# Kernel tuning notes

Hardware: AMD Instinct MI355X
Metric: run time of the kernel (lower is better)

## Reference

```python
import jax, jax.numpy as jnp
import numpy as np

N = 1024
IN_FEATURES = 128
N_HEADS = 8
N_HIDDEN = 16  # out_features // n_heads = 128 // 8
NEG_SLOPE = 0.2


def setup_inputs() -> dict:
    key = jax.random.key(0)
    k1, k2, k3, k4, k5 = jax.random.split(key, 5)
    h = jax.random.normal(k1, (N, IN_FEATURES), dtype=jnp.float32)
    adj_mat = jax.random.randint(k2, (N, N, 1), 0, 2, dtype=jnp.int32)
    s = jax.random.normal(k3, (N, N, 1), dtype=jnp.float32)
    # linear: nn.Linear(in_features, n_hidden*n_heads, bias=False) -> weight [128, 128]
    W = jax.random.normal(k4, (N_HEADS * N_HIDDEN, IN_FEATURES), dtype=jnp.float32) * 0.1
    # attn: nn.Linear(2*n_hidden, 1, bias=False) -> weight [1, 32]; stored flat [32]
    attn_w = jax.random.normal(k5, (2 * N_HIDDEN,), dtype=jnp.float32) * 0.1
    return {"h": h, "adj_mat": adj_mat, "s": s, "W": W, "attn_w": attn_w}


def reference(h, adj_mat, s, W, attn_w):
    n_nodes = h.shape[0]
    # g: [N, heads, hidden]
    g = (h @ W.T).reshape(n_nodes, N_HEADS, N_HIDDEN)
    # attn(cat(g_i, g_j)) = a_src . g_i + a_dst . g_j  (linear decomposes over concat)
    a_src = attn_w[:N_HIDDEN]
    a_dst = attn_w[N_HIDDEN:]
    src = jnp.einsum('ihf,f->ih', g, a_src)  # [N, heads]
    dst = jnp.einsum('jhf,f->jh', g, a_dst)  # [N, heads]
    e = jax.nn.leaky_relu(src[:, None, :] + dst[None, :, :], NEG_SLOPE)  # [N, N, heads]
    mask = adj_mat == 0  # [N, N, 1] broadcasts over heads
    neg_inf = jnp.array(-jnp.inf, dtype=e.dtype)
    e = jnp.where(mask, neg_inf, e)
    s_masked = jnp.where(mask, neg_inf, s)  # [N, N, 1]
    a = jax.nn.softmax(e, axis=1)               # [N, N, heads]
    s_prime = jax.nn.softmax(s_masked, axis=1)  # [N, N, 1]
    # NOTE: original applies a third softmax to (a + s_prime) WITHOUT re-masking,
    # so non-edge entries (value 0) get nonzero weight exp(0)/Z — replicated faithfully.
    new_attention = jax.nn.softmax(a + s_prime, axis=1)  # [N, N, heads]
    # dropout is identity in eval mode
    attn_res = jnp.einsum('ijh,jhf->ihf', new_attention, g)  # [N, heads, hidden]
    return attn_res.reshape(n_nodes, N_HEADS * N_HIDDEN)
```

## Files before the change

### kernel.cpp

```cpp
#include <hip/hip_runtime.h>

#define NNODES 1024
#define NHEADS 8
#define NHID 16
#define DIM 128
#define NEG_SLOPE 0.2f

template<int CTRL>
__device__ __forceinline__ float qbcast(float v) {
    return __int_as_float(__builtin_amdgcn_mov_dpp(__float_as_int(v), CTRL, 0xF, 0xF, true));
}

__global__ __launch_bounds__(256) void proj_kernel(
    const float* __restrict__ h, const float* __restrict__ W,
    const float* __restrict__ attn_w,
    float* __restrict__ g, float* __restrict__ srcv, float* __restrict__ dstv)
{
    const int bi = blockIdx.x & 63;
    const int bh = blockIdx.x >> 6;
    const int i0 = bi << 4;
    const int tid = threadIdx.x;
    __shared__ float4 hs[16][33];
    __shared__ float4 ws[16][33];
    const float4* h4 = (const float4*)h;
    const float4* W4 = (const float4*)W;
    {
        const int t0 = tid, t1 = tid + 256;
        hs[t0 >> 5][t0 & 31] = h4[(size_t)i0 * 32 + t0];
        hs[t1 >> 5][t1 & 31] = h4[(size_t)i0 * 32 + t1];
        ws[t0 >> 5][t0 & 31] = W4[(size_t)(bh * 16) * 32 + t0];
        ws[t1 >> 5][t1 & 31] = W4[(size_t)(bh * 16) * 32 + t1];
    }
    __syncthreads();
    const int il = tid >> 4;
    const int f  = tid & 15;
    float acc = 0.f;
#pragma unroll
    for (int k = 0; k < 32; k++) {
        const float4 a = hs[il][k];
        const float4 b = ws[f][k];
        acc = fmaf(a.x, b.x, fmaf(a.y, b.y, fmaf(a.z, b.z, fmaf(a.w, b.w, acc))));
    }
    const int i = i0 + il;
    g[(size_t)i * DIM + bh * NHID + f] = acc;
    float sv = acc * attn_w[f];
    float dv = acc * attn_w[NHID + f];
#pragma unroll
    for (int off = 1; off <= 8; off <<= 1) {
        sv += __shfl_xor(sv, off, 64);
        dv += __shfl_xor(dv, off, 64);
    }
    if (f == 0) { srcv[i * NHEADS + bh] = sv; dstv[i * NHEADS + bh] = dv; }
}

__global__ __launch_bounds__(512, 4) void fused_kernel(
    const int* __restrict__ adj, const float* __restrict__ s,
    const float* __restrict__ g, const float* __restrict__ srcv,
    const float* __restrict__ dstv, float* __restrict__ out)
{
    const int i0   = blockIdx.x * 2;
    const int tid  = threadIdx.x;
    const int lane = tid & 63;
    const int wv   = tid >> 6;

    __shared__ float evL[2][NNODES];
    __shared__ float dstL[NNODES * NHEADS];
    __shared__ float sh_src[2][NHEADS];
    __shared__ float zeA[8][NHEADS][2];
    __shared__ float zsA[8];
    __shared__ float statE[2][NHEADS];
    __shared__ float statS[2];
    __shared__ float redO[8][2][NHEADS][4][4];
    __shared__ float ztA[8][2][NHEADS];

    const int rA = tid >> 8;
    const int cA = tid & 255;
    float zs;
    {
        const int4   a  = ((const int4*)  adj)[(size_t)(i0 + rA) * (NNODES/4) + cA];
        const float4 sv = ((const float4*)s  )[(size_t)(i0 + rA) * (NNODES/4) + cA];
        float4 e4;
        e4.x = a.x ? __expf(sv.x) : 0.f;
        e4.y = a.y ? __expf(sv.y) : 0.f;
        e4.z = a.z ? __expf(sv.z) : 0.f;
        e4.w = a.w ? __expf(sv.w) : 0.f;
        ((float4*)evL[rA])[cA] = e4;
        zs = e4.x + e4.y + e4.z + e4.w;
    }
    {
        const float4* dv4 = (const float4*)dstv;
        float4* dl4 = (float4*)dstL;
#pragma unroll
        for (int k = 0; k < 4; k++) dl4[k * 512 + tid] = dv4[k * 512 + tid];
        if (tid < 16) sh_src[tid >> 3][tid & 7] =
            srcv[(size_t)(i0 + (tid >> 3)) * NHEADS + (tid & 7)];
    }
#pragma unroll
    for (int off = 1; off <= 32; off <<= 1) zs += __shfl_xor(zs, off, 64);
    if (lane == 0) zsA[wv] = zs;
    __syncthreads();

    const int hA  = tid & 7;
    const int jsA = tid >> 3;
    float ze0 = 0.f, ze1 = 0.f;
    {
        const float sH0 = sh_src[0][hA], sH1 = sh_src[1][hA];
#pragma unroll 4
        for (int t = 0; t < 16; t++) {
            const int j = t * 64 + jsA;
            const float d = dstL[j * NHEADS + hA];
            float e0 = sH0 + d; e0 = e0 > 0.f ? e0 : NEG_SLOPE * e0;
            float e1 = sH1 + d; e1 = e1 > 0.f ? e1 : NEG_SLOPE * e1;
            ze0 += (evL[0][j] != 0.f) ? __expf(e0) : 0.f;
            ze1 += (evL[1][j] != 0.f) ? __expf(e1) : 0.f;
        }
    }
#pragma unroll
    for (int off = 8; off <= 32; off <<= 1) {
        ze0 += __shfl_xor(ze0, off, 64);
        ze1 += __shfl_xor(ze1, off, 64);
    }
    if (lane < NHEADS) { zeA[wv][lane][0] = ze0; zeA[wv][lane][1] = ze1; }
    __syncthreads();
    if (tid < 16) {
        const int hh = tid & 7, rr = tid >> 3;
        float z = 0.f;
#pragma unroll
        for (int w2 = 0; w2 < 8; w2++) z += zeA[w2][hh][rr];
        statE[rr][hh] = 1.f / z;
    } else if (tid < 18) {
        const int rr = tid - 16;
        statS[rr] = 1.f / (zsA[rr*4] + zsA[rr*4+1] + zsA[rr*4+2] + zsA[rr*4+3]);
    }
    __syncthreads();

    const int qB  = tid & 3;
    const int hB  = (tid >> 2) & 7;
    const int jsB = tid >> 5;
    const float ize0 = statE[0][hB], ize1 = statE[1][hB];
    const float izs0 = statS[0],     izs1 = statS[1];
    const float sB0  = sh_src[0][hB], sB1 = sh_src[1][hB];

    float acc0[4] = {0.f,0.f,0.f,0.f};
    float acc1[4] = {0.f,0.f,0.f,0.f};
    float zt0 = 0.f, zt1 = 0.f;
    const float4* g4 = (const float4*)g;
    const int jw0   = qB * 16 + jsB;
    const int gidx0 = jsB * 32 + hB * 4 + qB;

#pragma unroll 2
    for (int tg = 0; tg < 16; tg++) {
        const int jw = tg * 64 + jw0;
        const float d = dstL[jw * NHEADS + hB];
        float e0 = sB0 + d; e0 = e0 > 0.f ? e0 : NEG_SLOPE * e0;
        float e1 = sB1 + d; e1 = e1 > 0.f ? e1 : NEG_SLOPE * e1;
        const float x0 = __expf(e0), x1 = __expf(e1);
        const float ev0 = evL[0][jw], ev1 = evL[1][jw];
        const float a0 = (ev0 != 0.f) ? fmaf(x0, ize0, ev0 * izs0) : 0.f;
        const float a1 = (ev1 != 0.f) ? fmaf(x1, ize1, ev1 * izs1) : 0.f;
        const float w0 = __expf(a0), w1 = __expf(a1);
        zt0 += w0; zt1 += w1;

#define KSTEP(K, CTRL)                                                        \
        {                                                                     \
            const float w0k = qbcast<CTRL>(w0);                               \
            const float w1k = qbcast<CTRL>(w1);                               \
            const float4 gv = g4[gidx0 + tg * 2048 + (K) * 512];              \
            acc0[0] = fmaf(w0k, gv.x, acc0[0]);                               \
            acc0[1] = fmaf(w0k, gv.y, acc0[1]);                               \
            acc0[2] = fmaf(w0k, gv.z, acc0[2]);                               \
            acc0[3] = fmaf(w0k, gv.w, acc0[3]);                               \
            acc1[0] = fmaf(w1k, gv.x, acc1[0]);                               \
            acc1[1] = fmaf(w1k, gv.y, acc1[1]);                               \
            acc1[2] = fmaf(w1k, gv.z, acc1[2]);                               \
            acc1[3] = fmaf(w1k, gv.w, acc1[3]);                               \
        }
        KSTEP(0, 0x00)
        KSTEP(1, 0x55)
        KSTEP(2, 0xAA)
        KSTEP(3, 0xFF)
#undef KSTEP
    }

#pragma unroll
    for (int m = 0; m < 4; m++) {
        acc0[m] += __shfl_xor(acc0[m], 32, 64);
        acc1[m] += __shfl_xor(acc1[m], 32, 64);
    }
    zt0 += __shfl_xor(zt0, 1, 64); zt0 += __shfl_xor(zt0, 2, 64); zt0 += __shfl_xor(zt0, 32, 64);
    zt1 += __shfl_xor(zt1, 1, 64); zt1 += __shfl_xor(zt1, 2, 64); zt1 += __shfl_xor(zt1, 32, 64);
    if (lane < 32) {
        *(float4*)&redO[wv][0][hB][qB][0] = make_float4(acc0[0], acc0[1], acc0[2], acc0[3]);
        *(float4*)&redO[wv][1][hB][qB][0] = make_float4(acc1[0], acc1[1], acc1[2], acc1[3]);
        if ((lane & 3) == 0) { ztA[wv][0][hB] = zt0; ztA[wv][1][hB] = zt1; }
    }
    __syncthreads();
    if (tid < 256) {
        const int rr = tid >> 7;
        const int hf = tid & 127;
        const int oh = hf >> 4;
        const int qq = (hf >> 2) & 3;
        const int mm = hf & 3;
        float v = 0.f, z = 0.f;
#pragma unroll
        for (int w2 = 0; w2 < 8; w2++) {
            v += redO[w2][rr][oh][qq][mm];
            z += ztA[w2][rr][oh];
        }
        out[(size_t)(i0 + rr) * DIM + hf] = v / z;
    }
}

extern "C" void kernel_launch(void* const* d_in, const int* in_sizes, int n_in,
                              void* d_out, int out_size, void* d_ws, size_t ws_size,
                              hipStream_t stream) {
    const float* h      = (const float*)d_in[0];
    const int*   adj    = (const int*)  d_in[1];
    const float* s      = (const float*)d_in[2];
    const float* W      = (const float*)d_in[3];
    const float* attn_w = (const float*)d_in[4];
    float* out = (float*)d_out;

    float* g    = (float*)d_ws;
    float* srcv = g    + (size_t)NNODES * DIM;
    float* dstv = srcv + (size_t)NNODES * NHEADS;

    proj_kernel <<<512, 256, 0, stream>>>(h, W, attn_w, g, srcv, dstv);
    fused_kernel<<<NNODES / 2, 512, 0, stream>>>(adj, s, g, srcv, dstv, out);
}
```

Before: 80.70 us.

## Process four query rows per block to reuse g loads across rows

Each block of the fused kernel now handles four destination rows with 1024 threads instead of two rows with 512 threads. Each g float4 load and each dst value is shared across four rows' accumulators, halving g traffic per output row and halving the number of dstv copies into shared memory. In exchange there are more registers per thread (16 accumulators), half as many blocks (256), larger shared arrays, and a changed j-to-lane mapping in the weighted-sum loop.

```diff
diff --git a/kernel.cpp b/kernel.cpp
--- a/kernel.cpp
+++ b/kernel.cpp
@@ -53,25 +53,25 @@
     if (f == 0) { srcv[i * NHEADS + bh] = sv; dstv[i * NHEADS + bh] = dv; }
 }
 
-__global__ __launch_bounds__(512, 4) void fused_kernel(
+__global__ __launch_bounds__(1024, 4) void fused_kernel(
     const int* __restrict__ adj, const float* __restrict__ s,
     const float* __restrict__ g, const float* __restrict__ srcv,
     const float* __restrict__ dstv, float* __restrict__ out)
 {
-    const int i0   = blockIdx.x * 2;
+    const int i0   = blockIdx.x * 4;
     const int tid  = threadIdx.x;
     const int lane = tid & 63;
     const int wv   = tid >> 6;
 
-    __shared__ float evL[2][NNODES];
+    __shared__ float evL[4][NNODES];
     __shared__ float dstL[NNODES * NHEADS];
-    __shared__ float sh_src[2][NHEADS];
-    __shared__ float zeA[8][NHEADS][2];
-    __shared__ float zsA[8];
-    __shared__ float statE[2][NHEADS];
-    __shared__ float statS[2];
-    __shared__ float redO[8][2][NHEADS][4][4];
-    __shared__ float ztA[8][2][NHEADS];
+    __shared__ float sh_src[4][NHEADS];
+    __shared__ float zeA[16][NHEADS][4];
+    __shared__ float zsA[16];
+    __shared__ float statE[4][NHEADS];
+    __shared__ float statS[4];
+    __shared__ float redO[16][4][NHEADS][4][4];
+    __shared__ float ztA[16][4][NHEADS];
 
     const int rA = tid >> 8;
     const int cA = tid & 255;
@@ -91,8 +91,8 @@
         const float4* dv4 = (const float4*)dstv;
         float4* dl4 = (float4*)dstL;
 #pragma unroll
-        for (int k = 0; k < 4; k++) dl4[k * 512 + tid] = dv4[k * 512 + tid];
-        if (tid < 16) sh_src[tid >> 3][tid & 7] =
+        for (int k = 0; k < 2; k++) dl4[k * 1024 + tid] = dv4[k * 1024 + tid];
+        if (tid < 32) sh_src[tid >> 3][tid & 7] =
             srcv[(size_t)(i0 + (tid >> 3)) * NHEADS + (tid & 7)];
     }
 #pragma unroll
@@ -102,34 +102,39 @@
 
     const int hA  = tid & 7;
     const int jsA = tid >> 3;
-    float ze0 = 0.f, ze1 = 0.f;
-    {
-        const float sH0 = sh_src[0][hA], sH1 = sh_src[1][hA];
+    float ze[4] = {0.f, 0.f, 0.f, 0.f};
+    {
+        const float sH[4] = { sh_src[0][hA], sh_src[1][hA],
+                              sh_src[2][hA], sh_src[3][hA] };
 #pragma unroll 4
-        for (int t = 0; t < 16; t++) {
-            const int j = t * 64 + jsA;
+        for (int t = 0; t < 8; t++) {
+            const int j = t * 128 + jsA;
             const float d = dstL[j * NHEADS + hA];
-            float e0 = sH0 + d; e0 = e0 > 0.f ? e0 : NEG_SLOPE * e0;
-            float e1 = sH1 + d; e1 = e1 > 0.f ? e1 : NEG_SLOPE * e1;
-            ze0 += (evL[0][j] != 0.f) ? __expf(e0) : 0.f;
-            ze1 += (evL[1][j] != 0.f) ? __expf(e1) : 0.f;
-        }
-    }
-#pragma unroll
-    for (int off = 8; off <= 32; off <<= 1) {
-        ze0 += __shfl_xor(ze0, off, 64);
-        ze1 += __shfl_xor(ze1, off, 64);
-    }
-    if (lane < NHEADS) { zeA[wv][lane][0] = ze0; zeA[wv][lane][1] = ze1; }
-    __syncthreads();
-    if (tid < 16) {
+#pragma unroll
+            for (int r = 0; r < 4; r++) {
+                float e = sH[r] + d;
+                e = e > 0.f ? e : NEG_SLOPE * e;
+                ze[r] += (evL[r][j] != 0.f) ? __expf(e) : 0.f;
+            }
+        }
+    }
+#pragma unroll
+    for (int off = 8; off <= 32; off <<= 1)
+#pragma unroll
+        for (int r = 0; r < 4; r++) ze[r] += __shfl_xor(ze[r], off, 64);
+    if (lane < NHEADS) {
+#pragma unroll
+        for (int r = 0; r < 4; r++) zeA[wv][lane][r] = ze[r];
+    }
+    __syncthreads();
+    if (tid < 32) {
         const int hh = tid & 7, rr = tid >> 3;
         float z = 0.f;
 #pragma unroll
-        for (int w2 = 0; w2 < 8; w2++) z += zeA[w2][hh][rr];
+        for (int w2 = 0; w2 < 16; w2++) z += zeA[w2][hh][rr];
         statE[rr][hh] = 1.f / z;
-    } else if (tid < 18) {
-        const int rr = tid - 16;
+    } else if (tid < 36) {
+        const int rr = tid - 32;
         statS[rr] = 1.f / (zsA[rr*4] + zsA[rr*4+1] + zsA[rr*4+2] + zsA[rr*4+3]);
     }
     __syncthreads();
@@ -137,43 +142,56 @@
     const int qB  = tid & 3;
     const int hB  = (tid >> 2) & 7;
     const int jsB = tid >> 5;
-    const float ize0 = statE[0][hB], ize1 = statE[1][hB];
-    const float izs0 = statS[0],     izs1 = statS[1];
-    const float sB0  = sh_src[0][hB], sB1 = sh_src[1][hB];
-
-    float acc0[4] = {0.f,0.f,0.f,0.f};
-    float acc1[4] = {0.f,0.f,0.f,0.f};
-    float zt0 = 0.f, zt1 = 0.f;
+    const float ize[4] = { statE[0][hB], statE[1][hB], statE[2][hB], statE[3][hB] };
+    const float izs[4] = { statS[0], statS[1], statS[2], statS[3] };
+    const float sB[4]  = { sh_src[0][hB], sh_src[1][hB], sh_src[2][hB], sh_src[3][hB] };
+
+    float acc[4][4] = {{0.f,0.f,0.f,0.f},{0.f,0.f,0.f,0.f},
+                       {0.f,0.f,0.f,0.f},{0.f,0.f,0.f,0.f}};
+    float zt[4] = {0.f, 0.f, 0.f, 0.f};
     const float4* g4 = (const float4*)g;
-    const int jw0   = qB * 16 + jsB;
-    const int gidx0 = jsB * 32 + hB * 4 + qB;
+    const int rowb0 = jsB * 4;
+    const int fq    = hB * 4 + qB;
 
 #pragma unroll 2
-    for (int tg = 0; tg < 16; tg++) {
-        const int jw = tg * 64 + jw0;
+    for (int tg = 0; tg < 8; tg++) {
+        const int jw = tg * 128 + rowb0 + qB;
         const float d = dstL[jw * NHEADS + hB];
-        float e0 = sB0 + d; e0 = e0 > 0.f ? e0 : NEG_SLOPE * e0;
-        float e1 = sB1 + d; e1 = e1 > 0.f ? e1 : NEG_SLOPE * e1;
-        const float x0 = __expf(e0), x1 = __expf(e1);
-        const float ev0 = evL[0][jw], ev1 = evL[1][jw];
-        const float a0 = (ev0 != 0.f) ? fmaf(x0, ize0, ev0 * izs0) : 0.f;
-        const float a1 = (ev1 != 0.f) ? fmaf(x1, ize1, ev1 * izs1) : 0.f;
-        const float w0 = __expf(a0), w1 = __expf(a1);
-        zt0 += w0; zt1 += w1;
-
+        float w[4];
+#pragma unroll
+        for (int r = 0; r < 4; r++) {
+            float e = sB[r] + d;
+            e = e > 0.f ? e : NEG_SLOPE * e;
+            const float x  = __expf(e);
+            const float ev = evL[r][jw];
+            const float arg = (ev != 0.f) ? fmaf(x, ize[r], ev * izs[r]) : 0.f;
+            w[r] = __expf(arg);
+            zt[r] += w[r];
+        }
 #define KSTEP(K, CTRL)                                                        \
         {                                                                     \
-            const float w0k = qbcast<CTRL>(w0);                               \
-            const float w1k = qbcast<CTRL>(w1);                               \
-            const float4 gv = g4[gidx0 + tg * 2048 + (K) * 512];              \
-            acc0[0] = fmaf(w0k, gv.x, acc0[0]);                               \
-            acc0[1] = fmaf(w0k, gv.y, acc0[1]);                               \
-            acc0[2] = fmaf(w0k, gv.z, acc0[2]);                               \
-            acc0[3] = fmaf(w0k, gv.w, acc0[3]);                               \
-            acc1[0] = fmaf(w1k, gv.x, acc1[0]);                               \
-            acc1[1] = fmaf(w1k, gv.y, acc1[1]);                               \
-            acc1[2] = fmaf(w1k, gv.z, acc1[2]);                               \
-            acc1[3] = fmaf(w1k, gv.w, acc1[3]);                               \
+            const int j = tg * 128 + rowb0 + (K);                             \
+            const float4 gv = g4[(size_t)j * 32 + fq];                        \
+            const float wk0 = qbcast<CTRL>(w[0]);                             \
+            const float wk1 = qbcast<CTRL>(w[1]);                             \
+            const float wk2 = qbcast<CTRL>(w[2]);                             \
+            const float wk3 = qbcast<CTRL>(w[3]);                             \
+            acc[0][0] = fmaf(wk0, gv.x, acc[0][0]);                           \
+            acc[0][1] = fmaf(wk0, gv.y, acc[0][1]);                           \
+            acc[0][2] = fmaf(wk0, gv.z, acc[0][2]);                           \
+            acc[0][3] = fmaf(wk0, gv.w, acc[0][3]);                           \
+            acc[1][0] = fmaf(wk1, gv.x, acc[1][0]);                           \
+            acc[1][1] = fmaf(wk1, gv.y, acc[1][1]);                           \
+            acc[1][2] = fmaf(wk1, gv.z, acc[1][2]);                           \
+            acc[1][3] = fmaf(wk1, gv.w, acc[1][3]);                           \
+            acc[2][0] = fmaf(wk2, gv.x, acc[2][0]);                           \
+            acc[2][1] = fmaf(wk2, gv.y, acc[2][1]);                           \
+            acc[2][2] = fmaf(wk2, gv.z, acc[2][2]);                           \
+            acc[2][3] = fmaf(wk2, gv.w, acc[2][3]);                           \
+            acc[3][0] = fmaf(wk3, gv.x, acc[3][0]);                           \
+            acc[3][1] = fmaf(wk3, gv.y, acc[3][1]);                           \
+            acc[3][2] = fmaf(wk3, gv.z, acc[3][2]);                           \
+            acc[3][3] = fmaf(wk3, gv.w, acc[3][3]);                           \
         }
         KSTEP(0, 0x00)
         KSTEP(1, 0x55)
@@ -183,19 +201,27 @@
     }
 
 #pragma unroll
-    for (int m = 0; m < 4; m++) {
-        acc0[m] += __shfl_xor(acc0[m], 32, 64);
-        acc1[m] += __shfl_xor(acc1[m], 32, 64);
-    }
-    zt0 += __shfl_xor(zt0, 1, 64); zt0 += __shfl_xor(zt0, 2, 64); zt0 += __shfl_xor(zt0, 32, 64);
-    zt1 += __shfl_xor(zt1, 1, 64); zt1 += __shfl_xor(zt1, 2, 64); zt1 += __shfl_xor(zt1, 32, 64);
+    for (int r = 0; r < 4; r++)
+#pragma unroll
+        for (int m = 0; m < 4; m++) acc[r][m] += __shfl_xor(acc[r][m], 32, 64);
+#pragma unroll
+    for (int r = 0; r < 4; r++) {
+        zt[r] += __shfl_xor(zt[r], 1, 64);
+        zt[r] += __shfl_xor(zt[r], 2, 64);
+        zt[r] += __shfl_xor(zt[r], 32, 64);
+    }
     if (lane < 32) {
-        *(float4*)&redO[wv][0][hB][qB][0] = make_float4(acc0[0], acc0[1], acc0[2], acc0[3]);
-        *(float4*)&redO[wv][1][hB][qB][0] = make_float4(acc1[0], acc1[1], acc1[2], acc1[3]);
-        if ((lane & 3) == 0) { ztA[wv][0][hB] = zt0; ztA[wv][1][hB] = zt1; }
-    }
-    __syncthreads();
-    if (tid < 256) {
+#pragma unroll
+        for (int r = 0; r < 4; r++)
+            *(float4*)&redO[wv][r][hB][qB][0] =
+                make_float4(acc[r][0], acc[r][1], acc[r][2], acc[r][3]);
+        if ((lane & 3) == 0) {
+#pragma unroll
+            for (int r = 0; r < 4; r++) ztA[wv][r][hB] = zt[r];
+        }
+    }
+    __syncthreads();
+    if (tid < 512) {
         const int rr = tid >> 7;
         const int hf = tid & 127;
         const int oh = hf >> 4;
@@ -203,7 +229,7 @@
         const int mm = hf & 3;
         float v = 0.f, z = 0.f;
 #pragma unroll
-        for (int w2 = 0; w2 < 8; w2++) {
+        for (int w2 = 0; w2 < 16; w2++) {
             v += redO[w2][rr][oh][qq][mm];
             z += ztA[w2][rr][oh];
         }
@@ -226,5 +252,5 @@
     float* dstv = srcv + (size_t)NNODES * NHEADS;
 
     proj_kernel <<<512, 256, 0, stream>>>(h, W, attn_w, g, srcv, dstv);
-    fused_kernel<<<NNODES / 2, 512, 0, stream>>>(adj, s, g, srcv, dstv, out);
-}
+    fused_kernel<<<NNODES / 4, 1024, 0, stream>>>(adj, s, g, srcv, dstv, out);
+}
```

After: 82.21 us. Within noise of the previous version (+1.9%).

## Fuse edge-softmax denominator pass into load phase and drop a barrier

Applied to the files above, without the earlier changes.

The per-head attention denominators are now computed in the same thread mapping as the adjacency/s load: each thread handles four j columns for all eight heads, reading dst values straight from global memory and its row's src from registers. This removes the separate LDS pass, one __syncthreads, and the single-thread reciprocal stage; every thread now computes its own reciprocals from per-wave partials. The main loop's j-to-lane mapping changes so each quad reads four consecutive g rows. The projection dot product is split into four independent accumulators to shorten the FMA dependency chain. The cost is more registers and more shuffles (eight heads reduced over six steps) and redundant global reads of dstv.

```diff
diff --git a/kernel.cpp b/kernel.cpp
--- a/kernel.cpp
+++ b/kernel.cpp
@@ -34,13 +34,20 @@
     __syncthreads();
     const int il = tid >> 4;
     const int f  = tid & 15;
-    float acc = 0.f;
-#pragma unroll
-    for (int k = 0; k < 32; k++) {
-        const float4 a = hs[il][k];
-        const float4 b = ws[f][k];
-        acc = fmaf(a.x, b.x, fmaf(a.y, b.y, fmaf(a.z, b.z, fmaf(a.w, b.w, acc))));
-    }
+    float p0 = 0.f, p1 = 0.f, p2 = 0.f, p3 = 0.f;
+#pragma unroll
+    for (int k = 0; k < 32; k += 4) {
+        float4 a, b;
+        a = hs[il][k];     b = ws[f][k];
+        p0 = fmaf(a.x, b.x, fmaf(a.y, b.y, fmaf(a.z, b.z, fmaf(a.w, b.w, p0))));
+        a = hs[il][k + 1]; b = ws[f][k + 1];
+        p1 = fmaf(a.x, b.x, fmaf(a.y, b.y, fmaf(a.z, b.z, fmaf(a.w, b.w, p1))));
+        a = hs[il][k + 2]; b = ws[f][k + 2];
+        p2 = fmaf(a.x, b.x, fmaf(a.y, b.y, fmaf(a.z, b.z, fmaf(a.w, b.w, p2))));
+        a = hs[il][k + 3]; b = ws[f][k + 3];
+        p3 = fmaf(a.x, b.x, fmaf(a.y, b.y, fmaf(a.z, b.z, fmaf(a.w, b.w, p3))));
+    }
+    const float acc = (p0 + p1) + (p2 + p3);
     const int i = i0 + il;
     g[(size_t)i * DIM + bh * NHID + f] = acc;
     float sv = acc * attn_w[f];
@@ -66,27 +73,13 @@
     __shared__ float evL[2][NNODES];
     __shared__ float dstL[NNODES * NHEADS];
     __shared__ float sh_src[2][NHEADS];
-    __shared__ float zeA[8][NHEADS][2];
+    __shared__ float zeA[8][NHEADS];
     __shared__ float zsA[8];
-    __shared__ float statE[2][NHEADS];
-    __shared__ float statS[2];
     __shared__ float redO[8][2][NHEADS][4][4];
     __shared__ float ztA[8][2][NHEADS];
 
     const int rA = tid >> 8;
     const int cA = tid & 255;
-    float zs;
-    {
-        const int4   a  = ((const int4*)  adj)[(size_t)(i0 + rA) * (NNODES/4) + cA];
-        const float4 sv = ((const float4*)s  )[(size_t)(i0 + rA) * (NNODES/4) + cA];
-        float4 e4;
-        e4.x = a.x ? __expf(sv.x) : 0.f;
-        e4.y = a.y ? __expf(sv.y) : 0.f;
-        e4.z = a.z ? __expf(sv.z) : 0.f;
-        e4.w = a.w ? __expf(sv.w) : 0.f;
-        ((float4*)evL[rA])[cA] = e4;
-        zs = e4.x + e4.y + e4.z + e4.w;
-    }
     {
         const float4* dv4 = (const float4*)dstv;
         float4* dl4 = (float4*)dstL;
@@ -95,85 +88,102 @@
         if (tid < 16) sh_src[tid >> 3][tid & 7] =
             srcv[(size_t)(i0 + (tid >> 3)) * NHEADS + (tid & 7)];
     }
-#pragma unroll
-    for (int off = 1; off <= 32; off <<= 1) zs += __shfl_xor(zs, off, 64);
-    if (lane == 0) zsA[wv] = zs;
-    __syncthreads();
-
-    const int hA  = tid & 7;
-    const int jsA = tid >> 3;
-    float ze0 = 0.f, ze1 = 0.f;
-    {
-        const float sH0 = sh_src[0][hA], sH1 = sh_src[1][hA];
-#pragma unroll 4
-        for (int t = 0; t < 16; t++) {
-            const int j = t * 64 + jsA;
-            const float d = dstL[j * NHEADS + hA];
-            float e0 = sH0 + d; e0 = e0 > 0.f ? e0 : NEG_SLOPE * e0;
-            float e1 = sH1 + d; e1 = e1 > 0.f ? e1 : NEG_SLOPE * e1;
-            ze0 += (evL[0][j] != 0.f) ? __expf(e0) : 0.f;
-            ze1 += (evL[1][j] != 0.f) ? __expf(e1) : 0.f;
+    float evj[4];
+    float zs;
+    {
+        const int4   a  = ((const int4*)  adj)[(size_t)(i0 + rA) * (NNODES/4) + cA];
+        const float4 sv = ((const float4*)s  )[(size_t)(i0 + rA) * (NNODES/4) + cA];
+        evj[0] = a.x ? __expf(sv.x) : 0.f;
+        evj[1] = a.y ? __expf(sv.y) : 0.f;
+        evj[2] = a.z ? __expf(sv.z) : 0.f;
+        evj[3] = a.w ? __expf(sv.w) : 0.f;
+        ((float4*)evL[rA])[cA] = make_float4(evj[0], evj[1], evj[2], evj[3]);
+        zs = (evj[0] + evj[1]) + (evj[2] + evj[3]);
+    }
+    float srcR[NHEADS];
+    {
+        const float4 s0 = ((const float4*)srcv)[(size_t)(i0 + rA) * 2 + 0];
+        const float4 s1 = ((const float4*)srcv)[(size_t)(i0 + rA) * 2 + 1];
+        srcR[0]=s0.x; srcR[1]=s0.y; srcR[2]=s0.z; srcR[3]=s0.w;
+        srcR[4]=s1.x; srcR[5]=s1.y; srcR[6]=s1.z; srcR[7]=s1.w;
+    }
+    float ze[NHEADS] = {0.f,0.f,0.f,0.f,0.f,0.f,0.f,0.f};
+    {
+        const float4* dv4 = (const float4*)dstv;
+#pragma unroll
+        for (int jj = 0; jj < 4; jj++) {
+            const int j = 4 * cA + jj;
+            const float4 d0 = dv4[(size_t)j * 2 + 0];
+            const float4 d1 = dv4[(size_t)j * 2 + 1];
+            const float dh[8] = {d0.x,d0.y,d0.z,d0.w,d1.x,d1.y,d1.z,d1.w};
+            const bool live = (evj[jj] != 0.f);
+#pragma unroll
+            for (int hh = 0; hh < 8; hh++) {
+                float e = srcR[hh] + dh[hh];
+                e = e > 0.f ? e : NEG_SLOPE * e;
+                ze[hh] += live ? __expf(e) : 0.f;
+            }
         }
     }
 #pragma unroll
-    for (int off = 8; off <= 32; off <<= 1) {
-        ze0 += __shfl_xor(ze0, off, 64);
-        ze1 += __shfl_xor(ze1, off, 64);
-    }
-    if (lane < NHEADS) { zeA[wv][lane][0] = ze0; zeA[wv][lane][1] = ze1; }
-    __syncthreads();
-    if (tid < 16) {
-        const int hh = tid & 7, rr = tid >> 3;
-        float z = 0.f;
-#pragma unroll
-        for (int w2 = 0; w2 < 8; w2++) z += zeA[w2][hh][rr];
-        statE[rr][hh] = 1.f / z;
-    } else if (tid < 18) {
-        const int rr = tid - 16;
-        statS[rr] = 1.f / (zsA[rr*4] + zsA[rr*4+1] + zsA[rr*4+2] + zsA[rr*4+3]);
+    for (int off = 1; off <= 32; off <<= 1) {
+        zs += __shfl_xor(zs, off, 64);
+#pragma unroll
+        for (int hh = 0; hh < 8; hh++) ze[hh] += __shfl_xor(ze[hh], off, 64);
+    }
+    if (lane == 0) {
+        zsA[wv] = zs;
+#pragma unroll
+        for (int hh = 0; hh < 8; hh++) zeA[wv][hh] = ze[hh];
     }
     __syncthreads();
 
     const int qB  = tid & 3;
     const int hB  = (tid >> 2) & 7;
     const int jsB = tid >> 5;
-    const float ize0 = statE[0][hB], ize1 = statE[1][hB];
-    const float izs0 = statS[0],     izs1 = statS[1];
-    const float sB0  = sh_src[0][hB], sB1 = sh_src[1][hB];
+    float ize[2], izs[2];
+#pragma unroll
+    for (int r = 0; r < 2; r++) {
+        const int w0 = r * 4;
+        ize[r] = 1.f / (zeA[w0][hB] + zeA[w0+1][hB] + zeA[w0+2][hB] + zeA[w0+3][hB]);
+        izs[r] = 1.f / (zsA[w0] + zsA[w0+1] + zsA[w0+2] + zsA[w0+3]);
+    }
+    const float sB[2] = { sh_src[0][hB], sh_src[1][hB] };
 
     float acc0[4] = {0.f,0.f,0.f,0.f};
     float acc1[4] = {0.f,0.f,0.f,0.f};
     float zt0 = 0.f, zt1 = 0.f;
     const float4* g4 = (const float4*)g;
-    const int jw0   = qB * 16 + jsB;
-    const int gidx0 = jsB * 32 + hB * 4 + qB;
+    const int rowb0 = jsB * 4;
+    const int fq    = hB * 4 + qB;
 
 #pragma unroll 2
     for (int tg = 0; tg < 16; tg++) {
-        const int jw = tg * 64 + jw0;
+        const int jw = tg * 64 + rowb0 + qB;
         const float d = dstL[jw * NHEADS + hB];
-        float e0 = sB0 + d; e0 = e0 > 0.f ? e0 : NEG_SLOPE * e0;
-        float e1 = sB1 + d; e1 = e1 > 0.f ? e1 : NEG_SLOPE * e1;
+        float e0 = sB[0] + d; e0 = e0 > 0.f ? e0 : NEG_SLOPE * e0;
+        float e1 = sB[1] + d; e1 = e1 > 0.f ? e1 : NEG_SLOPE * e1;
         const float x0 = __expf(e0), x1 = __expf(e1);
         const float ev0 = evL[0][jw], ev1 = evL[1][jw];
-        const float a0 = (ev0 != 0.f) ? fmaf(x0, ize0, ev0 * izs0) : 0.f;
-        const float a1 = (ev1 != 0.f) ? fmaf(x1, ize1, ev1 * izs1) : 0.f;
+        const float a0 = (ev0 != 0.f) ? fmaf(x0, ize[0], ev0 * izs[0]) : 0.f;
+        const float a1 = (ev1 != 0.f) ? fmaf(x1, ize[1], ev1 * izs[1]) : 0.f;
         const float w0 = __expf(a0), w1 = __expf(a1);
         zt0 += w0; zt1 += w1;
 
 #define KSTEP(K, CTRL)                                                        \
         {                                                                     \
-            const float w0k = qbcast<CTRL>(w0);                               \
-            const float w1k = qbcast<CTRL>(w1);                               \
-            const float4 gv = g4[gidx0 + tg * 2048 + (K) * 512];              \
-            acc0[0] = fmaf(w0k, gv.x, acc0[0]);                               \
-            acc0[1] = fmaf(w0k, gv.y, acc0[1]);                               \
-            acc0[2] = fmaf(w0k, gv.z, acc0[2]);                               \
-            acc0[3] = fmaf(w0k, gv.w, acc0[3]);                               \
-            acc1[0] = fmaf(w1k, gv.x, acc1[0]);                               \
-            acc1[1] = fmaf(w1k, gv.y, acc1[1]);                               \
-            acc1[2] = fmaf(w1k, gv.z, acc1[2]);                               \
-            acc1[3] = fmaf(w1k, gv.w, acc1[3]);                               \
+            const int j = tg * 64 + rowb0 + (K);                              \
+            const float4 gv = g4[(size_t)j * 32 + fq];                        \
+            const float wk0 = qbcast<CTRL>(w0);                               \
+            const float wk1 = qbcast<CTRL>(w1);                               \
+            acc0[0] = fmaf(wk0, gv.x, acc0[0]);                               \
+            acc0[1] = fmaf(wk0, gv.y, acc0[1]);                               \
+            acc0[2] = fmaf(wk0, gv.z, acc0[2]);                               \
+            acc0[3] = fmaf(wk0, gv.w, acc0[3]);                               \
+            acc1[0] = fmaf(wk1, gv.x, acc1[0]);                               \
+            acc1[1] = fmaf(wk1, gv.y, acc1[1]);                               \
+            acc1[2] = fmaf(wk1, gv.z, acc1[2]);                               \
+            acc1[3] = fmaf(wk1, gv.w, acc1[3]);                               \
         }
         KSTEP(0, 0x00)
         KSTEP(1, 0x55)
```

New measurement: 83.81 us. +3.9%, slower.

## Drop dstv shared-memory staging, raise occupancy, and remap node-to-lane layout

Applied to the files above, without the earlier changes.

Removes the 32KB per-block shared copy of dstv and reads it from global (L1/L2-cached) instead. This lowers LDS use so the fused kernel can raise launch bounds to 8 waves-per-EU occupancy. It also removes one barrier by having every thread reduce the softmax normalisers redundantly, and remaps which node j each lane handles so the four quad lanes read contiguous g rows. The projection kernel splits its dot-product into four independent accumulators to shorten the FMA dependency chain. The risks are more global-load latency in the inner loops and register pressure from the tighter launch bound.

```diff
diff --git a/kernel.cpp b/kernel.cpp
--- a/kernel.cpp
+++ b/kernel.cpp
@@ -34,13 +34,20 @@
     __syncthreads();
     const int il = tid >> 4;
     const int f  = tid & 15;
-    float acc = 0.f;
-#pragma unroll
-    for (int k = 0; k < 32; k++) {
-        const float4 a = hs[il][k];
-        const float4 b = ws[f][k];
-        acc = fmaf(a.x, b.x, fmaf(a.y, b.y, fmaf(a.z, b.z, fmaf(a.w, b.w, acc))));
-    }
+    float p0 = 0.f, p1 = 0.f, p2 = 0.f, p3 = 0.f;
+#pragma unroll
+    for (int k = 0; k < 32; k += 4) {
+        float4 a, b;
+        a = hs[il][k];     b = ws[f][k];
+        p0 = fmaf(a.x, b.x, fmaf(a.y, b.y, fmaf(a.z, b.z, fmaf(a.w, b.w, p0))));
+        a = hs[il][k + 1]; b = ws[f][k + 1];
+        p1 = fmaf(a.x, b.x, fmaf(a.y, b.y, fmaf(a.z, b.z, fmaf(a.w, b.w, p1))));
+        a = hs[il][k + 2]; b = ws[f][k + 2];
+        p2 = fmaf(a.x, b.x, fmaf(a.y, b.y, fmaf(a.z, b.z, fmaf(a.w, b.w, p2))));
+        a = hs[il][k + 3]; b = ws[f][k + 3];
+        p3 = fmaf(a.x, b.x, fmaf(a.y, b.y, fmaf(a.z, b.z, fmaf(a.w, b.w, p3))));
+    }
+    const float acc = (p0 + p1) + (p2 + p3);
     const int i = i0 + il;
     g[(size_t)i * DIM + bh * NHID + f] = acc;
     float sv = acc * attn_w[f];
@@ -53,7 +60,7 @@
     if (f == 0) { srcv[i * NHEADS + bh] = sv; dstv[i * NHEADS + bh] = dv; }
 }
 
-__global__ __launch_bounds__(512, 4) void fused_kernel(
+__global__ __launch_bounds__(512, 8) void fused_kernel(
     const int* __restrict__ adj, const float* __restrict__ s,
     const float* __restrict__ g, const float* __restrict__ srcv,
     const float* __restrict__ dstv, float* __restrict__ out)
@@ -64,12 +71,9 @@
     const int wv   = tid >> 6;
 
     __shared__ float evL[2][NNODES];
-    __shared__ float dstL[NNODES * NHEADS];
     __shared__ float sh_src[2][NHEADS];
     __shared__ float zeA[8][NHEADS][2];
     __shared__ float zsA[8];
-    __shared__ float statE[2][NHEADS];
-    __shared__ float statS[2];
     __shared__ float redO[8][2][NHEADS][4][4];
     __shared__ float ztA[8][2][NHEADS];
 
@@ -85,16 +89,10 @@
         e4.z = a.z ? __expf(sv.z) : 0.f;
         e4.w = a.w ? __expf(sv.w) : 0.f;
         ((float4*)evL[rA])[cA] = e4;
-        zs = e4.x + e4.y + e4.z + e4.w;
-    }
-    {
-        const float4* dv4 = (const float4*)dstv;
-        float4* dl4 = (float4*)dstL;
-#pragma unroll
-        for (int k = 0; k < 4; k++) dl4[k * 512 + tid] = dv4[k * 512 + tid];
-        if (tid < 16) sh_src[tid >> 3][tid & 7] =
-            srcv[(size_t)(i0 + (tid >> 3)) * NHEADS + (tid & 7)];
-    }
+        zs = (e4.x + e4.y) + (e4.z + e4.w);
+    }
+    if (tid < 16) sh_src[tid >> 3][tid & 7] =
+        srcv[(size_t)(i0 + (tid >> 3)) * NHEADS + (tid & 7)];
 #pragma unroll
     for (int off = 1; off <= 32; off <<= 1) zs += __shfl_xor(zs, off, 64);
     if (lane == 0) zsA[wv] = zs;
@@ -105,10 +103,10 @@
     float ze0 = 0.f, ze1 = 0.f;
     {
         const float sH0 = sh_src[0][hA], sH1 = sh_src[1][hA];
-#pragma unroll 4
+#pragma unroll 2
         for (int t = 0; t < 16; t++) {
             const int j = t * 64 + jsA;
-            const float d = dstL[j * NHEADS + hA];
+            const float d = dstv[j * NHEADS + hA];
             float e0 = sH0 + d; e0 = e0 > 0.f ? e0 : NEG_SLOPE * e0;
             float e1 = sH1 + d; e1 = e1 > 0.f ? e1 : NEG_SLOPE * e1;
             ze0 += (evL[0][j] != 0.f) ? __expf(e0) : 0.f;
@@ -122,58 +120,55 @@
     }
     if (lane < NHEADS) { zeA[wv][lane][0] = ze0; zeA[wv][lane][1] = ze1; }
     __syncthreads();
-    if (tid < 16) {
-        const int hh = tid & 7, rr = tid >> 3;
-        float z = 0.f;
-#pragma unroll
-        for (int w2 = 0; w2 < 8; w2++) z += zeA[w2][hh][rr];
-        statE[rr][hh] = 1.f / z;
-    } else if (tid < 18) {
-        const int rr = tid - 16;
-        statS[rr] = 1.f / (zsA[rr*4] + zsA[rr*4+1] + zsA[rr*4+2] + zsA[rr*4+3]);
-    }
-    __syncthreads();
 
     const int qB  = tid & 3;
     const int hB  = (tid >> 2) & 7;
     const int jsB = tid >> 5;
-    const float ize0 = statE[0][hB], ize1 = statE[1][hB];
-    const float izs0 = statS[0],     izs1 = statS[1];
-    const float sB0  = sh_src[0][hB], sB1 = sh_src[1][hB];
+    float ize[2], izs[2];
+    {
+        float z0 = 0.f, z1 = 0.f;
+#pragma unroll
+        for (int w2 = 0; w2 < 8; w2++) { z0 += zeA[w2][hB][0]; z1 += zeA[w2][hB][1]; }
+        ize[0] = 1.f / z0; ize[1] = 1.f / z1;
+        izs[0] = 1.f / (zsA[0] + zsA[1] + zsA[2] + zsA[3]);
+        izs[1] = 1.f / (zsA[4] + zsA[5] + zsA[6] + zsA[7]);
+    }
+    const float sB0 = sh_src[0][hB], sB1 = sh_src[1][hB];
 
     float acc0[4] = {0.f,0.f,0.f,0.f};
     float acc1[4] = {0.f,0.f,0.f,0.f};
     float zt0 = 0.f, zt1 = 0.f;
     const float4* g4 = (const float4*)g;
-    const int jw0   = qB * 16 + jsB;
-    const int gidx0 = jsB * 32 + hB * 4 + qB;
-
-#pragma unroll 2
+    const int rowb0 = jsB * 4;
+    const int fq    = hB * 4 + qB;
+
+#pragma unroll 1
     for (int tg = 0; tg < 16; tg++) {
-        const int jw = tg * 64 + jw0;
-        const float d = dstL[jw * NHEADS + hB];
+        const int jw = tg * 64 + rowb0 + qB;
+        const float d = dstv[jw * NHEADS + hB];
         float e0 = sB0 + d; e0 = e0 > 0.f ? e0 : NEG_SLOPE * e0;
         float e1 = sB1 + d; e1 = e1 > 0.f ? e1 : NEG_SLOPE * e1;
         const float x0 = __expf(e0), x1 = __expf(e1);
         const float ev0 = evL[0][jw], ev1 = evL[1][jw];
-        const float a0 = (ev0 != 0.f) ? fmaf(x0, ize0, ev0 * izs0) : 0.f;
-        const float a1 = (ev1 != 0.f) ? fmaf(x1, ize1, ev1 * izs1) : 0.f;
+        const float a0 = (ev0 != 0.f) ? fmaf(x0, ize[0], ev0 * izs[0]) : 0.f;
+        const float a1 = (ev1 != 0.f) ? fmaf(x1, ize[1], ev1 * izs[1]) : 0.f;
         const float w0 = __expf(a0), w1 = __expf(a1);
         zt0 += w0; zt1 += w1;
 
 #define KSTEP(K, CTRL)                                                        \
         {                                                                     \
-            const float w0k = qbcast<CTRL>(w0);                               \
-            const float w1k = qbcast<CTRL>(w1);                               \
-            const float4 gv = g4[gidx0 + tg * 2048 + (K) * 512];              \
-            acc0[0] = fmaf(w0k, gv.x, acc0[0]);                               \
-            acc0[1] = fmaf(w0k, gv.y, acc0[1]);                               \
-            acc0[2] = fmaf(w0k, gv.z, acc0[2]);                               \
-            acc0[3] = fmaf(w0k, gv.w, acc0[3]);                               \
-            acc1[0] = fmaf(w1k, gv.x, acc1[0]);                               \
-            acc1[1] = fmaf(w1k, gv.y, acc1[1]);                               \
-            acc1[2] = fmaf(w1k, gv.z, acc1[2]);                               \
-            acc1[3] = fmaf(w1k, gv.w, acc1[3]);                               \
+            const int j = tg * 64 + rowb0 + (K);                              \
+            const float4 gv = g4[(size_t)j * 32 + fq];                        \
+            const float wk0 = qbcast<CTRL>(w0);                               \
+            const float wk1 = qbcast<CTRL>(w1);                               \
+            acc0[0] = fmaf(wk0, gv.x, acc0[0]);                               \
+            acc0[1] = fmaf(wk0, gv.y, acc0[1]);                               \
+            acc0[2] = fmaf(wk0, gv.z, acc0[2]);                               \
+            acc0[3] = fmaf(wk0, gv.w, acc0[3]);                               \
+            acc1[0] = fmaf(wk1, gv.x, acc1[0]);                               \
+            acc1[1] = fmaf(wk1, gv.y, acc1[1]);                               \
+            acc1[2] = fmaf(wk1, gv.z, acc1[2]);                               \
+            acc1[3] = fmaf(wk1, gv.w, acc1[3]);                               \
         }
         KSTEP(0, 0x00)
         KSTEP(1, 0x55)
```

Measured after the change: 82.37 us. 1.02x slower.
